# Kernel optimization log

Measured on AMD Instinct MI355X. Metric: run time of the kernel, lower is better.

Reference implementation:

```python
import jax, jax.numpy as jnp
import numpy as np


def _maxpool(x, k):
    # NCHW max pool with window k, stride k, no padding
    return jax.lax.reduce_window(
        x, -jnp.inf, jax.lax.max,
        window_dimensions=(1, 1, k, k),
        window_strides=(1, 1, k, k),
        padding='VALID')


def setup_inputs() -> dict:
    key = jax.random.key(0)
    k1, k2, k3, k4, k5 = jax.random.split(key, 5)
    return {
        'input_tensor1': jax.random.normal(k1, (8, 128, 56, 56), dtype=jnp.float32),
        'input_tensor2': jax.random.normal(k2, (8, 64, 112, 112), dtype=jnp.float32),
        'input_tensor3': jax.random.normal(k3, (8, 32, 224, 224), dtype=jnp.float32),
        'input_tensor4': jax.random.normal(k4, (8, 16, 448, 448), dtype=jnp.float32),
        'pure_ff': jax.random.normal(k5, (8, 256, 28, 28), dtype=jnp.float32),
    }


def reference(input_tensor1, input_tensor2, input_tensor3, input_tensor4, pure_ff):
    # Original: cat input k times along channels, then maxpool. Pooling is
    # channel-independent, so pool-once-then-tile is mathematically identical
    # (the cat pattern [x,x,...,x] is an exact channel tiling).
    x1 = jnp.tile(_maxpool(input_tensor1, 2), (1, 2, 1, 1))
    x2 = jnp.tile(_maxpool(input_tensor2, 4), (1, 4, 1, 1))
    x3 = jnp.tile(_maxpool(input_tensor3, 8), (1, 8, 1, 1))
    x4 = jnp.tile(_maxpool(input_tensor4, 16), (1, 16, 1, 1))
    return jax.nn.relu(x1 + x2 + x3 + x4 + pure_ff)
```

## Files before the change

### kernel.cpp

```cpp
#include <hip/hip_runtime.h>

#define DEVINL __device__ __forceinline__

DEVINL float fmax4(float4 v) { return fmaxf(fmaxf(v.x, v.y), fmaxf(v.z, v.w)); }
DEVINL float4 max44(float4 a, float4 b) {
    float4 r; r.x = fmaxf(a.x, b.x); r.y = fmaxf(a.y, b.y);
    r.z = fmaxf(a.z, b.z); r.w = fmaxf(a.w, b.w); return r;
}

#define O1 0
#define O2 802816
#define O3 1204224
#define O4 1404928
#define WS_FLOATS 1505280

#define W_T4 3584
#define W_T3 10752
#define W_T2 14336
#define W_T1 21504

__global__ __launch_bounds__(256, 4) void pool_all(
    const float* __restrict__ t1, const float* __restrict__ t2,
    const float* __restrict__ t3, const float* __restrict__ t4,
    float* __restrict__ ws)
{
    __shared__ __align__(16) float scratch[4 * 448];
    const int tid  = threadIdx.x;
    const int lane = tid & 63;
    const int w    = blockIdx.x * 4 + (tid >> 6);
    float* sm = &scratch[(tid >> 6) * 448];

    if (w < W_T4) {
        const int ph = w % 28, cb = w / 28;
        const float* base = t4 + (size_t)cb * 200704 + ph * 7168;
        float4 acc[7];
        #pragma unroll
        for (int k = 0; k < 7; ++k)
            acc[k] = *(const float4*)(base + (k * 64 + lane) * 4);
        #pragma unroll
        for (int g = 1; g < 4; ++g) {
            float4 v[7];
            #pragma unroll
            for (int k = 0; k < 7; ++k)
                v[k] = *(const float4*)(base + g * 1792 + (k * 64 + lane) * 4);
            #pragma unroll
            for (int k = 0; k < 7; ++k) acc[k] = max44(acc[k], v[k]);
        }
        #pragma unroll
        for (int k = 0; k < 7; ++k) {
            const int p = k * 64 + lane;
            sm[(p / 112) * 112 + (p % 112)] = fmax4(acc[k]);
        }
    } else if (w < W_T3) {
        const int t = w - W_T4;
        const int ph = t % 28, cb = t / 28;
        const float* base = t3 + (size_t)cb * 50176 + ph * 1792;
        #pragma unroll
        for (int k = 0; k < 7; ++k) {
            float4 v = *(const float4*)(base + (k * 64 + lane) * 4);
            const int p = k * 64 + lane;
            sm[(p % 56) * 8 + (p / 56)] = fmax4(v);
        }
    } else if (w < W_T2) {
        const int t = w - W_T3;
        const int phq = t % 7, cb = t / 7;
        const float* base = t2 + (size_t)cb * 12544 + phq * 1792;
        #pragma unroll
        for (int k = 0; k < 7; ++k) {
            float4 v = *(const float4*)(base + (k * 64 + lane) * 4);
            const int p = k * 64 + lane;
            sm[(p % 28) * 16 + (p / 28)] = fmax4(v);
        }
    } else {
        const int t = w - W_T2;
        const int phq = t % 7, cb = t / 7;
        const float* base = t1 + (size_t)cb * 3136 + phq * 448;
        #pragma unroll
        for (int k = 0; k < 7; ++k) {
            const float v = base[k * 64 + lane];
            const int p = k * 64 + lane;
            sm[(p % 56) * 8 + (p / 56)] = v;
        }
    }

    __syncthreads();

    if (w < W_T4) {
        const int ph = w % 28, cb = w / 28;
        if (lane < 28) {
            float4 a = *(const float4*)&sm[0 * 112 + 4 * lane];
            float4 b = *(const float4*)&sm[1 * 112 + 4 * lane];
            float4 c = *(const float4*)&sm[2 * 112 + 4 * lane];
            float4 d = *(const float4*)&sm[3 * 112 + 4 * lane];
            ws[O4 + cb * 784 + ph * 28 + lane] =
                fmax4(max44(max44(a, b), max44(c, d)));
        }
    } else if (w < W_T3) {
        const int t = w - W_T4;
        const int ph = t % 28, cb = t / 28;
        if (lane < 28) {
            float4 a = *(const float4*)&sm[16 * lane + 0];
            float4 b = *(const float4*)&sm[16 * lane + 4];
            float4 c = *(const float4*)&sm[16 * lane + 8];
            float4 d = *(const float4*)&sm[16 * lane + 12];
            ws[O3 + cb * 784 + ph * 28 + lane] =
                fmax4(max44(max44(a, b), max44(c, d)));
        }
    } else if (w < W_T2) {
        const int t = w - W_T3;
        const int phq = t % 7, cb = t / 7;
        if (lane < 56) {
            #pragma unroll
            for (int h = 0; h < 2; ++h) {
                const int o = lane + h * 56;
                const int pr = o / 28, j = o % 28;
                float4 v = *(const float4*)&sm[j * 16 + pr * 4];
                ws[O2 + cb * 784 + phq * 112 + o] = fmax4(v);
            }
        }
    } else {
        const int t = w - W_T2;
        const int phq = t % 7, cb = t / 7;
        if (lane < 56) {
            #pragma unroll
            for (int h = 0; h < 2; ++h) {
                const int o = lane + h * 56;
                const int pr = o / 28, j = o % 28;
                float2 a = *(const float2*)&sm[16 * j + 2 * pr];
                float2 b = *(const float2*)&sm[16 * j + 8 + 2 * pr];
                ws[O1 + cb * 784 + phq * 112 + o] =
                    fmaxf(fmaxf(a.x, a.y), fmaxf(b.x, b.y));
            }
        }
    }
}

__global__ __launch_bounds__(256) void combine(
    const float* __restrict__ ws, const float* __restrict__ ff,
    float* __restrict__ out)
{
    const int i4 = blockIdx.x * 256 + threadIdx.x;
    const int pw4 = i4 % 7;
    const int ph  = (i4 / 7) % 28;
    const int c   = (i4 / 196) % 256;
    const int b   = i4 / 50176;
    const int ppw = ph * 7 + pw4;
    const float4* W = (const float4*)ws;
    float4 a1 = W[O1 / 4 + (b * 128 + (c & 127)) * 196 + ppw];
    float4 a2 = W[O2 / 4 + (b * 64  + (c & 63))  * 196 + ppw];
    float4 a3 = W[O3 / 4 + (b * 32  + (c & 31))  * 196 + ppw];
    float4 a4 = W[O4 / 4 + (b * 16  + (c & 15))  * 196 + ppw];
    float4 f  = ((const float4*)ff)[i4];
    float4 o;
    o.x = fmaxf(a1.x + a2.x + a3.x + a4.x + f.x, 0.0f);
    o.y = fmaxf(a1.y + a2.y + a3.y + a4.y + f.y, 0.0f);
    o.z = fmaxf(a1.z + a2.z + a3.z + a4.z + f.z, 0.0f);
    o.w = fmaxf(a1.w + a2.w + a3.w + a4.w + f.w, 0.0f);
    ((float4*)out)[i4] = o;
}

__global__ __launch_bounds__(256) void fused_pool_relu(
    const float* __restrict__ t1, const float* __restrict__ t2,
    const float* __restrict__ t3, const float* __restrict__ t4,
    const float* __restrict__ ff, float* __restrict__ out)
{
    const int pwq = blockIdx.x, ph = blockIdx.y, b = blockIdx.z;
    const int tid = threadIdx.x;
    const int pw0 = pwq * 4;
    __shared__ __align__(16) float p1[128 * 4];
    __shared__ __align__(16) float p2[64 * 4];
    __shared__ __align__(16) float p3[32 * 4];
    __shared__ __align__(16) float p4[16 * 4];
    {
        const int g = tid >> 4, l = tid & 15;
        const float* base = t4 + ((size_t)(b * 16 + g) * 448 + ph * 16) * 448
                          + pw0 * 16 + l * 4;
        float4 v[8];
        #pragma unroll
        for (int r = 0; r < 8; ++r) v[r] = *(const float4*)(base + r * 448);
        float4 acc = v[0];
        #pragma unroll
        for (int r = 1; r < 8; ++r) acc = max44(acc, v[r]);
        #pragma unroll
        for (int r = 8; r < 16; ++r) v[r - 8] = *(const float4*)(base + r * 448);
        #pragma unroll
        for (int r = 0; r < 8; ++r) acc = max44(acc, v[r]);
        float m = fmax4(acc);
        m = fmaxf(m, __shfl_xor(m, 1));
        m = fmaxf(m, __shfl_xor(m, 2));
        if ((l & 3) == 0) p4[g * 4 + (l >> 2)] = m;
    }
    {
        const int g = tid >> 3, l = tid & 7;
        const float* base = t3 + ((size_t)(b * 32 + g) * 224 + ph * 8) * 224
                          + pw0 * 8 + l * 4;
        float4 v[8];
        #pragma unroll
        for (int r = 0; r < 8; ++r) v[r] = *(const float4*)(base + r * 224);
        float4 acc = v[0];
        #pragma unroll
        for (int r = 1; r < 8; ++r) acc = max44(acc, v[r]);
        float m = fmax4(acc);
        m = fmaxf(m, __shfl_xor(m, 1));
        if ((l & 1) == 0) p3[g * 4 + (l >> 1)] = m;
    }
    {
        const int g = tid >> 2, l = tid & 3;
        const float* base = t2 + ((size_t)(b * 64 + g) * 112 + ph * 4) * 112
                          + pw0 * 4 + l * 4;
        float4 v[4];
        #pragma unroll
        for (int r = 0; r < 4; ++r) v[r] = *(const float4*)(base + r * 112);
        p2[g * 4 + l] = fmax4(max44(max44(v[0], v[1]), max44(v[2], v[3])));
    }
    {
        const int g = tid >> 1, l = tid & 1;
        const float* base = t1 + ((size_t)(b * 128 + g) * 56 + ph * 2) * 56
                          + pw0 * 2 + l * 4;
        float4 a = max44(*(const float4*)(base), *(const float4*)(base + 56));
        p1[g * 4 + l * 2 + 0] = fmaxf(a.x, a.y);
        p1[g * 4 + l * 2 + 1] = fmaxf(a.z, a.w);
    }
    __syncthreads();
    const int c = tid;
    const int o4 = (b * 200704 + c * 784 + ph * 28 + pw0) >> 2;
    const float4 f  = ((const float4*)ff)[o4];
    const float4 a1 = *(const float4*)&p1[(c & 127) * 4];
    const float4 a2 = *(const float4*)&p2[(c & 63) * 4];
    const float4 a3 = *(const float4*)&p3[(c & 31) * 4];
    const float4 a4 = *(const float4*)&p4[(c & 15) * 4];
    float4 o;
    o.x = fmaxf(a1.x + a2.x + a3.x + a4.x + f.x, 0.0f);
    o.y = fmaxf(a1.y + a2.y + a3.y + a4.y + f.y, 0.0f);
    o.z = fmaxf(a1.z + a2.z + a3.z + a4.z + f.z, 0.0f);
    o.w = fmaxf(a1.w + a2.w + a3.w + a4.w + f.w, 0.0f);
    ((float4*)out)[o4] = o;
}

extern "C" void kernel_launch(void* const* d_in, const int* in_sizes, int n_in,
                              void* d_out, int out_size, void* d_ws, size_t ws_size,
                              hipStream_t stream) {
    const float* t1 = (const float*)d_in[0];
    const float* t2 = (const float*)d_in[1];
    const float* t3 = (const float*)d_in[2];
    const float* t4 = (const float*)d_in[3];
    const float* ff = (const float*)d_in[4];
    float* out = (float*)d_out;

    if (ws_size >= (size_t)WS_FLOATS * sizeof(float)) {
        float* ws = (float*)d_ws;
        pool_all<<<W_T1 / 4, 256, 0, stream>>>(t1, t2, t3, t4, ws);
        combine<<<1568, 256, 0, stream>>>(ws, ff, out);
    } else {
        dim3 grid(7, 28, 8);
        fused_pool_relu<<<grid, 256, 0, stream>>>(t1, t2, t3, t4, ff, out);
    }
}
```

Measured before the change: 226.9 us.

## Drop block barrier in pool kernel and restructure per-wave loads and LDS layout

Each wave now loads, reduces and writes back through its own private LDS slice, separated only by compiler memory barriers, instead of the whole block meeting at __syncthreads. The 16x16 branch issues 14 float4 loads per batch to keep more memory requests in flight. Each branch also uses a simpler row-major LDS layout with new reduction indexing. The aim is to let waves proceed independently and hide more memory latency. The code now relies on LDS operations being ordered within a single wavefront, which holds in practice but is only enforced by the compiler barrier.

```diff
diff --git a/kernel.cpp b/kernel.cpp
--- a/kernel.cpp
+++ b/kernel.cpp
@@ -7,6 +7,8 @@
     float4 r; r.x = fmaxf(a.x, b.x); r.y = fmaxf(a.y, b.y);
     r.z = fmaxf(a.z, b.z); r.w = fmaxf(a.w, b.w); return r;
 }
+
+#define MEMBAR() asm volatile("" ::: "memory")
 
 #define O1 0
 #define O2 802816
@@ -32,61 +34,25 @@
 
     if (w < W_T4) {
         const int ph = w % 28, cb = w / 28;
-        const float* base = t4 + (size_t)cb * 200704 + ph * 7168;
-        float4 acc[7];
-        #pragma unroll
-        for (int k = 0; k < 7; ++k)
-            acc[k] = *(const float4*)(base + (k * 64 + lane) * 4);
-        #pragma unroll
-        for (int g = 1; g < 4; ++g) {
-            float4 v[7];
-            #pragma unroll
-            for (int k = 0; k < 7; ++k)
-                v[k] = *(const float4*)(base + g * 1792 + (k * 64 + lane) * 4);
-            #pragma unroll
-            for (int k = 0; k < 7; ++k) acc[k] = max44(acc[k], v[k]);
-        }
-        #pragma unroll
-        for (int k = 0; k < 7; ++k) {
-            const int p = k * 64 + lane;
-            sm[(p / 112) * 112 + (p % 112)] = fmax4(acc[k]);
-        }
-    } else if (w < W_T3) {
-        const int t = w - W_T4;
-        const int ph = t % 28, cb = t / 28;
-        const float* base = t3 + (size_t)cb * 50176 + ph * 1792;
-        #pragma unroll
-        for (int k = 0; k < 7; ++k) {
-            float4 v = *(const float4*)(base + (k * 64 + lane) * 4);
-            const int p = k * 64 + lane;
-            sm[(p % 56) * 8 + (p / 56)] = fmax4(v);
-        }
-    } else if (w < W_T2) {
-        const int t = w - W_T3;
-        const int phq = t % 7, cb = t / 7;
-        const float* base = t2 + (size_t)cb * 12544 + phq * 1792;
-        #pragma unroll
-        for (int k = 0; k < 7; ++k) {
-            float4 v = *(const float4*)(base + (k * 64 + lane) * 4);
-            const int p = k * 64 + lane;
-            sm[(p % 28) * 16 + (p / 28)] = fmax4(v);
-        }
-    } else {
-        const int t = w - W_T2;
-        const int phq = t % 7, cb = t / 7;
-        const float* base = t1 + (size_t)cb * 3136 + phq * 448;
-        #pragma unroll
-        for (int k = 0; k < 7; ++k) {
-            const float v = base[k * 64 + lane];
-            const int p = k * 64 + lane;
-            sm[(p % 56) * 8 + (p / 56)] = v;
-        }
-    }
-
-    __syncthreads();
-
-    if (w < W_T4) {
-        const int ph = w % 28, cb = w / 28;
+        const float* base = t4 + (size_t)cb * 200704 + ph * 7168 + 4 * lane;
+        float4 v[14], acc[7];
+        #pragma unroll
+        for (int k = 0; k < 7; ++k) v[k]     = *(const float4*)(base + k * 256);
+        #pragma unroll
+        for (int k = 0; k < 7; ++k) v[7 + k] = *(const float4*)(base + 1792 + k * 256);
+        MEMBAR();
+        #pragma unroll
+        for (int k = 0; k < 7; ++k) acc[k] = max44(v[k], v[7 + k]);
+        #pragma unroll
+        for (int k = 0; k < 7; ++k) v[k]     = *(const float4*)(base + 3584 + k * 256);
+        #pragma unroll
+        for (int k = 0; k < 7; ++k) v[7 + k] = *(const float4*)(base + 5376 + k * 256);
+        MEMBAR();
+        #pragma unroll
+        for (int k = 0; k < 7; ++k) acc[k] = max44(acc[k], max44(v[k], v[7 + k]));
+        #pragma unroll
+        for (int k = 0; k < 7; ++k) sm[k * 64 + lane] = fmax4(acc[k]);
+        MEMBAR();
         if (lane < 28) {
             float4 a = *(const float4*)&sm[0 * 112 + 4 * lane];
             float4 b = *(const float4*)&sm[1 * 112 + 4 * lane];
@@ -98,38 +64,66 @@
     } else if (w < W_T3) {
         const int t = w - W_T4;
         const int ph = t % 28, cb = t / 28;
+        const float* base = t3 + (size_t)cb * 50176 + ph * 1792 + 4 * lane;
+        float4 v[7];
+        #pragma unroll
+        for (int k = 0; k < 7; ++k) v[k] = *(const float4*)(base + k * 256);
+        MEMBAR();
+        #pragma unroll
+        for (int k = 0; k < 7; ++k) sm[k * 64 + lane] = fmax4(v[k]);
+        MEMBAR();
         if (lane < 28) {
-            float4 a = *(const float4*)&sm[16 * lane + 0];
-            float4 b = *(const float4*)&sm[16 * lane + 4];
-            float4 c = *(const float4*)&sm[16 * lane + 8];
-            float4 d = *(const float4*)&sm[16 * lane + 12];
-            ws[O3 + cb * 784 + ph * 28 + lane] =
-                fmax4(max44(max44(a, b), max44(c, d)));
+            float m = fmaxf(sm[2 * lane], sm[2 * lane + 1]);
+            #pragma unroll
+            for (int r = 1; r < 8; ++r)
+                m = fmaxf(m, fmaxf(sm[r * 56 + 2 * lane], sm[r * 56 + 2 * lane + 1]));
+            ws[O3 + cb * 784 + ph * 28 + lane] = m;
         }
     } else if (w < W_T2) {
         const int t = w - W_T3;
         const int phq = t % 7, cb = t / 7;
+        const float* base = t2 + (size_t)cb * 12544 + phq * 1792 + 4 * lane;
+        float4 v[7];
+        #pragma unroll
+        for (int k = 0; k < 7; ++k) v[k] = *(const float4*)(base + k * 256);
+        MEMBAR();
+        #pragma unroll
+        for (int k = 0; k < 7; ++k) sm[k * 64 + lane] = fmax4(v[k]);
+        MEMBAR();
         if (lane < 56) {
+            const int pr0 = lane / 28, pc = lane % 28;
             #pragma unroll
             for (int h = 0; h < 2; ++h) {
-                const int o = lane + h * 56;
-                const int pr = o / 28, j = o % 28;
-                float4 v = *(const float4*)&sm[j * 16 + pr * 4];
-                ws[O2 + cb * 784 + phq * 112 + o] = fmax4(v);
+                const int pr = pr0 + 2 * h;
+                float m = fmaxf(fmaxf(sm[(4 * pr + 0) * 28 + pc],
+                                      sm[(4 * pr + 1) * 28 + pc]),
+                                fmaxf(sm[(4 * pr + 2) * 28 + pc],
+                                      sm[(4 * pr + 3) * 28 + pc]));
+                ws[O2 + cb * 784 + phq * 112 + pr * 28 + pc] = m;
             }
         }
     } else {
         const int t = w - W_T2;
         const int phq = t % 7, cb = t / 7;
+        const float* base = t1 + (size_t)cb * 3136 + phq * 448;
         if (lane < 56) {
+            float4 a = *(const float4*)(base + 4 * lane);
+            float4 b = *(const float4*)(base + 224 + 4 * lane);
+            MEMBAR();
+            float2 ha; ha.x = fmaxf(a.x, a.y); ha.y = fmaxf(a.z, a.w);
+            float2 hb; hb.x = fmaxf(b.x, b.y); hb.y = fmaxf(b.z, b.w);
+            const int ra = lane / 14, c2 = lane % 14;
+            *(float2*)&sm[ra * 28 + 2 * c2]       = ha;
+            *(float2*)&sm[(ra + 4) * 28 + 2 * c2] = hb;
+        }
+        MEMBAR();
+        if (lane < 56) {
+            const int pr0 = lane / 28, j = lane % 28;
             #pragma unroll
             for (int h = 0; h < 2; ++h) {
-                const int o = lane + h * 56;
-                const int pr = o / 28, j = o % 28;
-                float2 a = *(const float2*)&sm[16 * j + 2 * pr];
-                float2 b = *(const float2*)&sm[16 * j + 8 + 2 * pr];
-                ws[O1 + cb * 784 + phq * 112 + o] =
-                    fmaxf(fmaxf(a.x, a.y), fmaxf(b.x, b.y));
+                const int pr = pr0 + 2 * h;
+                float m = fmaxf(sm[(2 * pr) * 28 + j], sm[(2 * pr + 1) * 28 + j]);
+                ws[O1 + cb * 784 + phq * 112 + pr * 28 + j] = m;
             }
         }
     }
```

After: 224.7 us. About the same (-0.9%).
